# Kernel optimization log

Hardware: AMD Instinct MI355X
Metric: run time of the kernel (lower is better)

The kernel has to match this reference:

```python
import jax, jax.numpy as jnp
import numpy as np

HEADS = 4
DIM_HEAD = 128

def setup_inputs() -> dict:
    key = jax.random.key(0)
    k1, k2, k3, k4 = jax.random.split(key, 4)
    scale = DIM_HEAD ** -0.5
    return {
        "fmap": jax.random.normal(k1, (16, 512, 32, 32), dtype=jnp.float32),
        "w_qkv": jax.random.normal(k2, (1536, 512), dtype=jnp.float32) * 0.02,
        "height": jax.random.normal(k3, (32, DIM_HEAD), dtype=jnp.float32) * scale,
        "width": jax.random.normal(k4, (32, DIM_HEAD), dtype=jnp.float32) * scale,
    }

def reference(fmap, w_qkv, height, width):
    b, c, h, w = fmap.shape
    scale = DIM_HEAD ** -0.5
    # 1x1 conv == channel GEMM: (b, 3*heads*dim_head, h, w)
    qkv = jnp.einsum('bchw,oc->bohw', fmap, w_qkv)
    # split into q,k,v and reshape to (b, heads, seq, dim_head)
    qkv = qkv.reshape(b, 3, HEADS, DIM_HEAD, h * w)
    q, k, v = (jnp.transpose(qkv[:, i], (0, 1, 3, 2)) for i in range(3))
    # content logits
    sim = jnp.einsum('bhid,bhjd->bhij', q, k) * scale
    # absolute positional bias: emb[(x,y)] = height[x] + width[y]
    emb = (height[:, None, :] + width[None, :, :]).reshape(h * w, DIM_HEAD)
    sim = sim + jnp.einsum('bhid,jd->bhij', q, emb) * scale
    attn = jax.nn.softmax(sim, axis=-1)
    out = jnp.einsum('bhij,bhjd->bhid', attn, v)  # (b, heads, seq, d)
    out = jnp.transpose(out, (0, 1, 3, 2)).reshape(b, HEADS * DIM_HEAD, h, w)
    return out
```

## Files before the change

kernel.cpp:

```cpp
#include <hip/hip_runtime.h>
#include <math.h>

#define HEADS 4
#define DIMH  128
#define NB    16
#define CIN   512
#define SEQ   1024
#define OTOT  1536
#define KQ    (CIN / 8)

typedef __attribute__((ext_vector_type(8)))  short bf16x8;
typedef __attribute__((ext_vector_type(4)))  short bf16x4;
typedef __attribute__((ext_vector_type(4)))  float f32x4;
typedef __attribute__((ext_vector_type(16))) float f32x16;

#define MFMA16(a,b,c) __builtin_amdgcn_mfma_f32_16x16x32_bf16(a,b,c,0,0,0)
#define MFMA32(a,b,c) __builtin_amdgcn_mfma_f32_32x32x16_bf16(a,b,c,0,0,0)

__device__ __forceinline__ short f2bf(float f) {
    unsigned u = __builtin_bit_cast(unsigned, f);
    u = (u + 0x7FFFu + ((u >> 16) & 1u)) >> 16;
    return (short)u;
}

__global__ __launch_bounds__(256) void convert_w(const float* __restrict__ W,
                                                 short* __restrict__ Wb2) {
    const int o  = blockIdx.x * 256 + threadIdx.x;
    const int kq = blockIdx.y;
    float4 v0 = *(const float4*)&W[(size_t)o * CIN + kq * 8];
    float4 v1 = *(const float4*)&W[(size_t)o * CIN + kq * 8 + 4];
    bf16x8 pk = { f2bf(v0.x), f2bf(v0.y), f2bf(v0.z), f2bf(v0.w),
                  f2bf(v1.x), f2bf(v1.y), f2bf(v1.z), f2bf(v1.w) };
    *(bf16x8*)&Wb2[((size_t)kq * OTOT + o) * 8] = pk;
}

__global__ __launch_bounds__(256) void convert_fmap(const float* __restrict__ F,
                                                    short* __restrict__ FT2) {
    const int s  = blockIdx.x * 256 + threadIdx.x;
    const int kq = blockIdx.y, b = blockIdx.z;
    const float* src = F + ((size_t)b * CIN + kq * 8) * SEQ + s;
    float v[8];
    #pragma unroll
    for (int i = 0; i < 8; ++i) v[i] = src[(size_t)i * SEQ];
    bf16x8 pk = { f2bf(v[0]), f2bf(v[1]), f2bf(v[2]), f2bf(v[3]),
                  f2bf(v[4]), f2bf(v[5]), f2bf(v[6]), f2bf(v[7]) };
    *(bf16x8*)&FT2[(((size_t)b * KQ + kq) * SEQ + s) * 8] = pk;
}

__global__ __launch_bounds__(256, 3) void qkv_gemm(
    const short* __restrict__ Wb2, const short* __restrict__ FT2,
    const float* __restrict__ height, const float* __restrict__ width,
    short* __restrict__ Qo, short* __restrict__ Ko, short* __restrict__ Vo)
{
    const int b = blockIdx.z, o0 = blockIdx.y * 128, s0 = blockIdx.x * 128;
    const int t = threadIdx.x, l = t & 63, w = t >> 6;
    const int quad = l >> 4, ln = l & 15;
    const int wrow = (w >> 1) * 64, wcol = (w & 1) * 64;

    const short* Ap = Wb2 + (((size_t)quad * OTOT) + (o0 + wrow + ln)) * 8;
    const short* Bp = FT2 + ((((size_t)b * KQ + quad) * SEQ) + (s0 + wcol + ln)) * 8;

    f32x4 acc[4][4] = {};

    #pragma unroll 2
    for (int ks = 0; ks < 16; ++ks) {
        bf16x8 af[4], bfr[4];
        const short* a = Ap + (size_t)ks * 4 * OTOT * 8;
        const short* bb = Bp + (size_t)ks * 4 * SEQ * 8;
        #pragma unroll
        for (int i = 0; i < 4; ++i) af[i] = *(const bf16x8*)(a + (size_t)i * 16 * 8);
        #pragma unroll
        for (int j = 0; j < 4; ++j) bfr[j] = *(const bf16x8*)(bb + (size_t)j * 16 * 8);
        #pragma unroll
        for (int i = 0; i < 4; ++i)
            #pragma unroll
            for (int j = 0; j < 4; ++j)
                acc[i][j] = MFMA16(af[i], bfr[j], acc[i][j]);
    }

    const int sec = o0 >> 9;
    const int h   = (o0 >> 7) & 3;
    const size_t bh = (size_t)b * HEADS + h;

    if (sec == 0) {
        const float qs = 0.08838834764831845f * 1.4426950408889634f;
        #pragma unroll
        for (int ti = 0; ti < 4; ++ti) {
            int d = wrow + ti * 16 + quad * 4;
            #pragma unroll
            for (int tj = 0; tj < 4; ++tj) {
                int s = s0 + wcol + tj * 16 + ln;
                f32x4 a = acc[ti][tj];
                bf16x4 pk = { f2bf(a[0] * qs), f2bf(a[1] * qs), f2bf(a[2] * qs), f2bf(a[3] * qs) };
                *(bf16x4*)&Qo[(bh * SEQ + s) * DIMH + d] = pk;
            }
        }
    } else if (sec == 1) {
        #pragma unroll
        for (int ti = 0; ti < 4; ++ti) {
            int d = wrow + ti * 16 + quad * 4;
            #pragma unroll
            for (int tj = 0; tj < 4; ++tj) {
                int s = s0 + wcol + tj * 16 + ln;
                float4 hv = *(const float4*)&height[(size_t)(s >> 5) * DIMH + d];
                float4 wv = *(const float4*)&width[(size_t)(s & 31) * DIMH + d];
                f32x4 a = acc[ti][tj];
                bf16x4 pk = { f2bf(a[0] + hv.x + wv.x), f2bf(a[1] + hv.y + wv.y),
                              f2bf(a[2] + hv.z + wv.z), f2bf(a[3] + hv.w + wv.w) };
                *(bf16x4*)&Ko[(bh * SEQ + s) * DIMH + d] = pk;
            }
        }
    } else {
        #pragma unroll
        for (int ti = 0; ti < 4; ++ti) {
            int d = wrow + ti * 16 + quad * 4;
            #pragma unroll
            for (int tj = 0; tj < 4; ++tj) {
                int s = s0 + wcol + tj * 16 + ln;
                f32x4 a = acc[ti][tj];
                #pragma unroll
                for (int r = 0; r < 4; ++r)
                    Vo[(bh * DIMH + d + r) * SEQ + s] = f2bf(a[r]);
            }
        }
    }
}

#define BQ 128
#define BJ 64
#define KSTR 136
#define VSTR 72
#define PSTR 72

__global__ __launch_bounds__(256, 2) void attn(
    const short* __restrict__ Q, const short* __restrict__ K,
    const short* __restrict__ V, float* __restrict__ out)
{
    __shared__ short Ks[BJ * KSTR];
    __shared__ short Vs[DIMH * VSTR];
    __shared__ short Ps[BQ * PSTR];
    __shared__ float ls[BQ];

    const int t = threadIdx.x, l = t & 63, w = t >> 6;
    const int h = l >> 5, c31 = l & 31;

    const int L = blockIdx.x;
    const int x = L & 7, inner = L >> 3;
    const int bh = x * 8 + (inner >> 3);
    const int q0 = (inner & 7) * BQ;
    const size_t base = (size_t)bh * DIMH * SEQ;

    bf16x8 qf[8];
    {
        const short* Qp = Q + base + (size_t)(q0 + w * 32 + c31) * DIMH + h * 8;
        #pragma unroll
        for (int kc = 0; kc < 8; ++kc)
            qf[kc] = *(const bf16x8*)(Qp + kc * 16);
    }

    f32x16 O[4] = {};
    f32x16 psum = {};

    for (int j0 = 0; j0 < SEQ; j0 += BJ) {
        __syncthreads();
        #pragma unroll
        for (int p = 0; p < 4; ++p) {
            int j = (w * 4 + p) * 4 + (l >> 4);
            int c8 = (l & 15) * 8;
            int4 v = *(const int4*)(K + base + (size_t)(j0 + j) * DIMH + c8);
            *(int4*)&Ks[j * KSTR + c8] = v;
        }
        #pragma unroll
        for (int p = 0; p < 4; ++p) {
            int d = (w * 4 + p) * 8 + (l >> 3);
            int j8 = (l & 7) * 8;
            int4 v = *(const int4*)(V + base + (size_t)d * SEQ + j0 + j8);
            *(int4*)&Vs[d * VSTR + j8] = v;
        }
        __syncthreads();

        f32x16 S0 = {}, S1 = {};
        #pragma unroll
        for (int kc = 0; kc < 8; ++kc) {
            bf16x8 k0 = *(const bf16x8*)&Ks[c31 * KSTR + kc * 16 + h * 8];
            bf16x8 k1 = *(const bf16x8*)&Ks[(32 + c31) * KSTR + kc * 16 + h * 8];
            S0 = MFMA32(qf[kc], k0, S0);
            S1 = MFMA32(qf[kc], k1, S1);
        }

        #pragma unroll
        for (int r = 0; r < 16; ++r) {
            float p0 = __builtin_amdgcn_exp2f(S0[r]);
            float p1 = __builtin_amdgcn_exp2f(S1[r]);
            psum[r] += p0 + p1;
            int i = w * 32 + (r & 3) + 8 * (r >> 2) + 4 * h;
            Ps[i * PSTR + c31]      = f2bf(p0);
            Ps[i * PSTR + 32 + c31] = f2bf(p1);
        }

        #pragma unroll
        for (int jc = 0; jc < 4; ++jc) {
            bf16x8 pf = *(const bf16x8*)&Ps[(w * 32 + c31) * PSTR + jc * 16 + h * 8];
            #pragma unroll
            for (int dc = 0; dc < 4; ++dc) {
                bf16x8 vf = *(const bf16x8*)&Vs[(dc * 32 + c31) * VSTR + jc * 16 + h * 8];
                O[dc] = MFMA32(vf, pf, O[dc]);
            }
        }
    }

    #pragma unroll
    for (int r = 0; r < 16; ++r) {
        float s = psum[r];
        #pragma unroll
        for (int m = 1; m < 32; m <<= 1) s += __shfl_xor(s, m);
        psum[r] = s;
    }
    if (c31 == 0) {
        #pragma unroll
        for (int r = 0; r < 16; ++r)
            ls[w * 32 + (r & 3) + 8 * (r >> 2) + 4 * h] = psum[r];
    }
    float linv = 1.0f / ls[w * 32 + c31];

    #pragma unroll
    for (int dc = 0; dc < 4; ++dc)
        #pragma unroll
        for (int r = 0; r < 16; ++r) {
            int d = dc * 32 + (r & 3) + 8 * (r >> 2) + 4 * h;
            out[base + (size_t)d * SEQ + q0 + w * 32 + c31] = O[dc][r] * linv;
        }
}

extern "C" void kernel_launch(void* const* d_in, const int* in_sizes, int n_in,
                              void* d_out, int out_size, void* d_ws, size_t ws_size,
                              hipStream_t stream) {
    const float* fmap   = (const float*)d_in[0];
    const float* w_qkv  = (const float*)d_in[1];
    const float* height = (const float*)d_in[2];
    const float* width  = (const float*)d_in[3];
    float* outp = (float*)d_out;

    const size_t n_ft  = (size_t)NB * SEQ * CIN;
    const size_t n_w   = (size_t)OTOT * CIN;
    const size_t n_qkv = (size_t)NB * HEADS * SEQ * DIMH;

    short* FT2 = (short*)d_ws;
    short* Wb2 = FT2 + n_ft;
    short* Qb  = Wb2 + n_w;
    short* Kb  = Qb + n_qkv;
    short* Vb  = Kb + n_qkv;

    convert_fmap<<<dim3(SEQ / 256, KQ, NB), 256, 0, stream>>>(fmap, FT2);
    convert_w<<<dim3(OTOT / 256, KQ), 256, 0, stream>>>(w_qkv, Wb2);
    qkv_gemm<<<dim3(SEQ / 128, OTOT / 128, NB), 256, 0, stream>>>(
        Wb2, FT2, height, width, Qb, Kb, Vb);
    attn<<<dim3(NB * HEADS * (SEQ / BQ)), 256, 0, stream>>>(Qb, Kb, Vb, outp);
}
```

Baseline: 177.9 us.

## Keep P in registers, read V fragments from pre-swizzled global layout, double-buffer K

The QKV GEMM now writes K in a d-chunked layout and V in an MFMA-fragment-ready layout. The attention kernel can then read V fragments straight from global memory and compute S transposed (K as the A operand), so the exp'd probabilities pack directly into B-operand registers. This removes the P and V shared-memory round trips. Row sums come from an MFMA against a ones vector instead of shuffles plus an LDS reduction. K tiles are double-buffered in LDS with register prefetch, leaving one barrier per tile, and the QKV GEMM gets explicit two-stage register prefetch. The cost is scattered 2-byte V stores in the GEMM epilogue and uncached global V reads that every wave repeats.

Result: slower. 196.8 us (+10.6%).

```diff
diff --git a/kernel.cpp b/kernel.cpp
--- a/kernel.cpp
+++ b/kernel.cpp
@@ -22,17 +22,11 @@
     u = (u + 0x7FFFu + ((u >> 16) & 1u)) >> 16;
     return (short)u;
 }
-
-__global__ __launch_bounds__(256) void convert_w(const float* __restrict__ W,
-                                                 short* __restrict__ Wb2) {
-    const int o  = blockIdx.x * 256 + threadIdx.x;
-    const int kq = blockIdx.y;
-    float4 v0 = *(const float4*)&W[(size_t)o * CIN + kq * 8];
-    float4 v1 = *(const float4*)&W[(size_t)o * CIN + kq * 8 + 4];
-    bf16x8 pk = { f2bf(v0.x), f2bf(v0.y), f2bf(v0.z), f2bf(v0.w),
-                  f2bf(v1.x), f2bf(v1.y), f2bf(v1.z), f2bf(v1.w) };
-    *(bf16x8*)&Wb2[((size_t)kq * OTOT + o) * 8] = pk;
-}
+__device__ __forceinline__ unsigned pk2(float lo, float hi) {
+    return __builtin_amdgcn_perm(__builtin_bit_cast(unsigned, hi),
+                                 __builtin_bit_cast(unsigned, lo), 0x07060302u);
+}
+union PF8 { unsigned u[4]; bf16x8 v; };
 
 __global__ __launch_bounds__(256) void convert_fmap(const float* __restrict__ F,
                                                     short* __restrict__ FT2) {
@@ -47,10 +41,21 @@
     *(bf16x8*)&FT2[(((size_t)b * KQ + kq) * SEQ + s) * 8] = pk;
 }
 
+__global__ __launch_bounds__(256) void convert_w(const float* __restrict__ W,
+                                                 short* __restrict__ Wb2) {
+    const int o  = blockIdx.x * 256 + threadIdx.x;
+    const int kq = blockIdx.y;
+    float4 v0 = *(const float4*)&W[(size_t)o * CIN + kq * 8];
+    float4 v1 = *(const float4*)&W[(size_t)o * CIN + kq * 8 + 4];
+    bf16x8 pk = { f2bf(v0.x), f2bf(v0.y), f2bf(v0.z), f2bf(v0.w),
+                  f2bf(v1.x), f2bf(v1.y), f2bf(v1.z), f2bf(v1.w) };
+    *(bf16x8*)&Wb2[((size_t)kq * OTOT + o) * 8] = pk;
+}
+
 __global__ __launch_bounds__(256, 3) void qkv_gemm(
     const short* __restrict__ Wb2, const short* __restrict__ FT2,
     const float* __restrict__ height, const float* __restrict__ width,
-    short* __restrict__ Qo, short* __restrict__ Ko, short* __restrict__ Vo)
+    short* __restrict__ Qo, short* __restrict__ Kfo, short* __restrict__ Vfo)
 {
     const int b = blockIdx.z, o0 = blockIdx.y * 128, s0 = blockIdx.x * 128;
     const int t = threadIdx.x, l = t & 63, w = t >> 6;
@@ -61,21 +66,25 @@
     const short* Bp = FT2 + ((((size_t)b * KQ + quad) * SEQ) + (s0 + wcol + ln)) * 8;
 
     f32x4 acc[4][4] = {};
-
-    #pragma unroll 2
-    for (int ks = 0; ks < 16; ++ks) {
-        bf16x8 af[4], bfr[4];
-        const short* a = Ap + (size_t)ks * 4 * OTOT * 8;
-        const short* bb = Bp + (size_t)ks * 4 * SEQ * 8;
-        #pragma unroll
-        for (int i = 0; i < 4; ++i) af[i] = *(const bf16x8*)(a + (size_t)i * 16 * 8);
-        #pragma unroll
-        for (int j = 0; j < 4; ++j) bfr[j] = *(const bf16x8*)(bb + (size_t)j * 16 * 8);
-        #pragma unroll
-        for (int i = 0; i < 4; ++i)
-            #pragma unroll
-            for (int j = 0; j < 4; ++j)
-                acc[i][j] = MFMA16(af[i], bfr[j], acc[i][j]);
+    bf16x8 a0[4], b0[4], a1[4], b1[4];
+
+#define GLOADF(ks, af, bfr) { \
+    const short* ga = Ap + (size_t)(ks) * 4 * OTOT * 8; \
+    const short* gb = Bp + (size_t)(ks) * 4 * SEQ * 8; \
+    _Pragma("unroll") for (int i = 0; i < 4; ++i) af[i]  = *(const bf16x8*)(ga + (size_t)i * 16 * 8); \
+    _Pragma("unroll") for (int j = 0; j < 4; ++j) bfr[j] = *(const bf16x8*)(gb + (size_t)j * 16 * 8); }
+#define COMP(af, bfr) { \
+    _Pragma("unroll") for (int i = 0; i < 4; ++i) \
+        _Pragma("unroll") for (int j = 0; j < 4; ++j) \
+            acc[i][j] = MFMA16(af[i], bfr[j], acc[i][j]); }
+
+    GLOADF(0, a0, b0);
+    GLOADF(1, a1, b1);
+    for (int ks = 0; ks < 16; ks += 2) {
+        COMP(a0, b0);
+        if (ks + 2 < 16) GLOADF(ks + 2, a0, b0);
+        COMP(a1, b1);
+        if (ks + 3 < 16) GLOADF(ks + 3, a1, b1);
     }
 
     const int sec = o0 >> 9;
@@ -91,8 +100,8 @@
             for (int tj = 0; tj < 4; ++tj) {
                 int s = s0 + wcol + tj * 16 + ln;
                 f32x4 a = acc[ti][tj];
-                bf16x4 pk = { f2bf(a[0] * qs), f2bf(a[1] * qs), f2bf(a[2] * qs), f2bf(a[3] * qs) };
-                *(bf16x4*)&Qo[(bh * SEQ + s) * DIMH + d] = pk;
+                bf16x4 pk4 = { f2bf(a[0]*qs), f2bf(a[1]*qs), f2bf(a[2]*qs), f2bf(a[3]*qs) };
+                *(bf16x4*)&Qo[(bh * SEQ + s) * DIMH + d] = pk4;
             }
         }
     } else if (sec == 1) {
@@ -105,22 +114,24 @@
                 float4 hv = *(const float4*)&height[(size_t)(s >> 5) * DIMH + d];
                 float4 wv = *(const float4*)&width[(size_t)(s & 31) * DIMH + d];
                 f32x4 a = acc[ti][tj];
-                bf16x4 pk = { f2bf(a[0] + hv.x + wv.x), f2bf(a[1] + hv.y + wv.y),
-                              f2bf(a[2] + hv.z + wv.z), f2bf(a[3] + hv.w + wv.w) };
-                *(bf16x4*)&Ko[(bh * SEQ + s) * DIMH + d] = pk;
+                bf16x4 pk4 = { f2bf(a[0] + hv.x + wv.x), f2bf(a[1] + hv.y + wv.y),
+                               f2bf(a[2] + hv.z + wv.z), f2bf(a[3] + hv.w + wv.w) };
+                *(bf16x4*)&Kfo[(((size_t)bh * 16 + (d >> 3)) * SEQ + s) * 8 + (d & 7)] = pk4;
             }
         }
     } else {
+        const int slot = ((ln >> 2) & 1) * 8 + (ln & 3) + ((ln >> 3) << 2);
         #pragma unroll
         for (int ti = 0; ti < 4; ++ti) {
             int d = wrow + ti * 16 + quad * 4;
             #pragma unroll
             for (int tj = 0; tj < 4; ++tj) {
                 int s = s0 + wcol + tj * 16 + ln;
+                size_t vb = (((size_t)bh * 64 + (s >> 4)) * DIMH) * 16 + slot;
                 f32x4 a = acc[ti][tj];
                 #pragma unroll
                 for (int r = 0; r < 4; ++r)
-                    Vo[(bh * DIMH + d + r) * SEQ + s] = f2bf(a[r]);
+                    Vfo[vb + (size_t)(d + r) * 16] = f2bf(a[r]);
             }
         }
     }
@@ -129,17 +140,12 @@
 #define BQ 128
 #define BJ 64
 #define KSTR 136
-#define VSTR 72
-#define PSTR 72
 
 __global__ __launch_bounds__(256, 2) void attn(
-    const short* __restrict__ Q, const short* __restrict__ K,
-    const short* __restrict__ V, float* __restrict__ out)
+    const short* __restrict__ Q, const short* __restrict__ Kf,
+    const short* __restrict__ Vf, float* __restrict__ out)
 {
-    __shared__ short Ks[BJ * KSTR];
-    __shared__ short Vs[DIMH * VSTR];
-    __shared__ short Ps[BQ * PSTR];
-    __shared__ float ls[BQ];
+    __shared__ short Ks[2 * BJ * KSTR];
 
     const int t = threadIdx.x, l = t & 63, w = t >> 6;
     const int h = l >> 5, c31 = l & 31;
@@ -148,87 +154,94 @@
     const int x = L & 7, inner = L >> 3;
     const int bh = x * 8 + (inner >> 3);
     const int q0 = (inner & 7) * BQ;
-    const size_t base = (size_t)bh * DIMH * SEQ;
+    const size_t obase = (size_t)bh * DIMH * SEQ;
 
     bf16x8 qf[8];
     {
-        const short* Qp = Q + base + (size_t)(q0 + w * 32 + c31) * DIMH + h * 8;
+        const short* Qp = Q + ((size_t)bh * SEQ + (q0 + w * 32 + c31)) * DIMH + h * 8;
         #pragma unroll
         for (int kc = 0; kc < 8; ++kc)
             qf[kc] = *(const bf16x8*)(Qp + kc * 16);
     }
 
+    PF8 ones;
+    ones.u[0] = ones.u[1] = ones.u[2] = ones.u[3] = 0x3F803F80u;
+
+    const short* Kg = Kf + (size_t)bh * 16 * SEQ * 8;
+    const short* Vlane = Vf + (size_t)bh * 64 * (DIMH * 16) + (c31 * 16 + h * 8);
+
     f32x16 O[4] = {};
-    f32x16 psum = {};
-
-    for (int j0 = 0; j0 < SEQ; j0 += BJ) {
+    f32x16 Lacc = {};
+
+    {
+        int4 kreg[4];
+        #pragma unroll
+        for (int p = 0; p < 4; ++p)
+            kreg[p] = *(const int4*)(Kg + ((size_t)(p * 4 + w) * SEQ + l) * 8);
+        #pragma unroll
+        for (int p = 0; p < 4; ++p)
+            *(int4*)&Ks[l * KSTR + (p * 4 + w) * 8] = kreg[p];
+    }
+    __syncthreads();
+
+    for (int ti = 0; ti < 16; ++ti) {
+        const int cur = (ti & 1) * (BJ * KSTR);
+        const int nxt = (BJ * KSTR) - cur;
+        int4 kreg[4];
+        if (ti < 15) {
+            const int j0n = (ti + 1) * BJ;
+            #pragma unroll
+            for (int p = 0; p < 4; ++p)
+                kreg[p] = *(const int4*)(Kg + ((size_t)(p * 4 + w) * SEQ + j0n + l) * 8);
+        }
+
+        f32x16 S0 = {}, S1 = {};
+        #pragma unroll
+        for (int kc = 0; kc < 8; ++kc) {
+            bf16x8 k0 = *(const bf16x8*)&Ks[cur + c31 * KSTR + kc * 16 + h * 8];
+            bf16x8 k1 = *(const bf16x8*)&Ks[cur + (32 + c31) * KSTR + kc * 16 + h * 8];
+            S0 = MFMA32(k0, qf[kc], S0);
+            S1 = MFMA32(k1, qf[kc], S1);
+        }
+
+        const int jgb = ti * 4;
+        #pragma unroll
+        for (int half = 0; half < 2; ++half) {
+            const f32x16& S = half ? S1 : S0;
+            #pragma unroll
+            for (int kk = 0; kk < 2; ++kk) {
+                PF8 pf;
+                #pragma unroll
+                for (int m = 0; m < 4; ++m) {
+                    float a = __builtin_amdgcn_exp2f(S[kk * 8 + 2 * m]);
+                    float b = __builtin_amdgcn_exp2f(S[kk * 8 + 2 * m + 1]);
+                    pf.u[m] = pk2(a, b);
+                }
+                Lacc = MFMA32(ones.v, pf.v, Lacc);
+                const short* vp = Vlane + (size_t)(jgb + half * 2 + kk) * (DIMH * 16);
+                #pragma unroll
+                for (int dc = 0; dc < 4; ++dc) {
+                    bf16x8 vf = *(const bf16x8*)(vp + dc * 32 * 16);
+                    O[dc] = MFMA32(vf, pf.v, O[dc]);
+                }
+            }
+        }
+
+        if (ti < 15) {
+            #pragma unroll
+            for (int p = 0; p < 4; ++p)
+                *(int4*)&Ks[nxt + l * KSTR + (p * 4 + w) * 8] = kreg[p];
+        }
         __syncthreads();
-        #pragma unroll
-        for (int p = 0; p < 4; ++p) {
-            int j = (w * 4 + p) * 4 + (l >> 4);
-            int c8 = (l & 15) * 8;
-            int4 v = *(const int4*)(K + base + (size_t)(j0 + j) * DIMH + c8);
-            *(int4*)&Ks[j * KSTR + c8] = v;
-        }
-        #pragma unroll
-        for (int p = 0; p < 4; ++p) {
-            int d = (w * 4 + p) * 8 + (l >> 3);
-            int j8 = (l & 7) * 8;
-            int4 v = *(const int4*)(V + base + (size_t)d * SEQ + j0 + j8);
-            *(int4*)&Vs[d * VSTR + j8] = v;
-        }
-        __syncthreads();
-
-        f32x16 S0 = {}, S1 = {};
-        #pragma unroll
-        for (int kc = 0; kc < 8; ++kc) {
-            bf16x8 k0 = *(const bf16x8*)&Ks[c31 * KSTR + kc * 16 + h * 8];
-            bf16x8 k1 = *(const bf16x8*)&Ks[(32 + c31) * KSTR + kc * 16 + h * 8];
-            S0 = MFMA32(qf[kc], k0, S0);
-            S1 = MFMA32(qf[kc], k1, S1);
-        }
-
-        #pragma unroll
-        for (int r = 0; r < 16; ++r) {
-            float p0 = __builtin_amdgcn_exp2f(S0[r]);
-            float p1 = __builtin_amdgcn_exp2f(S1[r]);
-            psum[r] += p0 + p1;
-            int i = w * 32 + (r & 3) + 8 * (r >> 2) + 4 * h;
-            Ps[i * PSTR + c31]      = f2bf(p0);
-            Ps[i * PSTR + 32 + c31] = f2bf(p1);
-        }
-
-        #pragma unroll
-        for (int jc = 0; jc < 4; ++jc) {
-            bf16x8 pf = *(const bf16x8*)&Ps[(w * 32 + c31) * PSTR + jc * 16 + h * 8];
-            #pragma unroll
-            for (int dc = 0; dc < 4; ++dc) {
-                bf16x8 vf = *(const bf16x8*)&Vs[(dc * 32 + c31) * VSTR + jc * 16 + h * 8];
-                O[dc] = MFMA32(vf, pf, O[dc]);
-            }
-        }
-    }
-
-    #pragma unroll
-    for (int r = 0; r < 16; ++r) {
-        float s = psum[r];
-        #pragma unroll
-        for (int m = 1; m < 32; m <<= 1) s += __shfl_xor(s, m);
-        psum[r] = s;
-    }
-    if (c31 == 0) {
-        #pragma unroll
-        for (int r = 0; r < 16; ++r)
-            ls[w * 32 + (r & 3) + 8 * (r >> 2) + 4 * h] = psum[r];
-    }
-    float linv = 1.0f / ls[w * 32 + c31];
-
+    }
+
+    float linv = 1.0f / Lacc[0];
     #pragma unroll
     for (int dc = 0; dc < 4; ++dc)
         #pragma unroll
         for (int r = 0; r < 16; ++r) {
             int d = dc * 32 + (r & 3) + 8 * (r >> 2) + 4 * h;
-            out[base + (size_t)d * SEQ + q0 + w * 32 + c31] = O[dc][r] * linv;
+            out[obase + (size_t)d * SEQ + q0 + w * 32 + c31] = O[dc][r] * linv;
         }
 }
 
@@ -248,12 +261,12 @@
     short* FT2 = (short*)d_ws;
     short* Wb2 = FT2 + n_ft;
     short* Qb  = Wb2 + n_w;
-    short* Kb  = Qb + n_qkv;
-    short* Vb  = Kb + n_qkv;
+    short* Kfb = Qb + n_qkv;
+    short* Vfb = Kfb + n_qkv;
 
     convert_fmap<<<dim3(SEQ / 256, KQ, NB), 256, 0, stream>>>(fmap, FT2);
     convert_w<<<dim3(OTOT / 256, KQ), 256, 0, stream>>>(w_qkv, Wb2);
     qkv_gemm<<<dim3(SEQ / 128, OTOT / 128, NB), 256, 0, stream>>>(
-        Wb2, FT2, height, width, Qb, Kb, Vb);
-    attn<<<dim3(NB * HEADS * (SEQ / BQ)), 256, 0, stream>>>(Qb, Kb, Vb, outp);
-}
+        Wb2, FT2, height, width, Qb, Kfb, Vfb);
+    attn<<<dim3(NB * HEADS * (SEQ / BQ)), 256, 0, stream>>>(Qb, Kfb, Vfb, outp);
+}
```
